# Optimization experiments

Hardware: AMD Instinct MI355X
Metric: run time of the kernel (lower is better)

The kernel has to match this reference:

```python
import jax, jax.numpy as jnp
import numpy as np

ALPHA = 0.2  # LeakyReLU negative slope
NEG_INF = -9e15  # matches torch -9000000000000000.0


def setup_inputs() -> dict:
    key = jax.random.key(0)
    k1, k2, k3, k4, k5, k6 = jax.random.split(key, 6)
    N, F_in, F_out = 4096, 512, 256
    adj = jax.random.randint(k1, (N, N), 0, 2, dtype=jnp.int32)
    h = jax.random.normal(k2, (N, F_in), dtype=jnp.float32)
    # proj: Linear(F_in, F_out)
    W = jax.random.normal(k3, (F_in, F_out), dtype=jnp.float32) * (1.0 / np.sqrt(F_in))
    b = jax.random.normal(k4, (F_out,), dtype=jnp.float32) * 0.01
    # proj_a: Linear(2*F_out, 1) split into the two halves acting on src/dst features
    a1 = jax.random.normal(k5, (F_out,), dtype=jnp.float32) * (1.0 / np.sqrt(2 * F_out))
    a2 = jax.random.normal(k6, (F_out,), dtype=jnp.float32) * (1.0 / np.sqrt(2 * F_out))
    a_b = jnp.zeros((), dtype=jnp.float32)
    return {"adj": adj, "h": h, "W": W, "b": b, "a1": a1, "a2": a2, "a_b": a_b}


def reference(adj, h, W, b, a1, a2, a_b):
    # wh = proj(h): [N, F_out]
    wh = h @ W + b
    # Fused form of the N x N x 2F concat + Linear(2F,1):
    # logits[i, j] = wh[i] . a1 + wh[j] . a2 + a_b
    f_src = wh @ a1  # [N]
    f_dst = wh @ a2  # [N]
    e = jax.nn.leaky_relu(f_src[:, None] + f_dst[None, :] + a_b, negative_slope=ALPHA)
    e = jnp.where(adj > 0, e, NEG_INF)
    att = jax.nn.softmax(e, axis=-1)  # F.softmax legacy dim=1 for 2D
    # dropout: inference mode (no-op) for deterministic reference
    out = att @ wh  # [N, F_out]
    return jax.nn.elu(out)  # concat=True
```

## Files before the change

kernel.cpp:

```cpp
#include <hip/hip_runtime.h>

#define NN   4096
#define FIN  512
#define FOUT 256
#define ALPHA 0.2f

typedef __attribute__((ext_vector_type(8))) short short8;
typedef __attribute__((ext_vector_type(4))) float f32x4;
typedef unsigned short u16;
typedef unsigned int u32;
typedef unsigned long long u64;

__device__ __forceinline__ u16 f2bf(float x) {
    union { float f; unsigned u; } v; v.f = x;
    unsigned r = v.u + 0x7FFF + ((v.u >> 16) & 1);
    return (u16)(r >> 16);
}

__global__ __launch_bounds__(256) void k_wt(const float* __restrict__ W,
                                            u16* __restrict__ Wt,
                                            float* __restrict__ fs,
                                            float* __restrict__ fd) {
    __shared__ float s[64 * 65];
    const int t  = threadIdx.x;
    const int g  = (blockIdx.y * gridDim.x + blockIdx.x) * 256 + t;
    if (g < NN) fs[g] = 0.f; else fd[g - NN] = 0.f;
    const int f0 = blockIdx.x * 64;
    const int k0 = blockIdx.y * 64;
    #pragma unroll
    for (int p = 0; p < 4; ++p) {
        int q = t + 256 * p, rr = q >> 4, cc = q & 15;
        float4 w4 = *(const float4*)&W[(size_t)(k0 + rr) * FOUT + f0 + cc * 4];
        s[(cc * 4 + 0) * 65 + rr] = w4.x;
        s[(cc * 4 + 1) * 65 + rr] = w4.y;
        s[(cc * 4 + 2) * 65 + rr] = w4.z;
        s[(cc * 4 + 3) * 65 + rr] = w4.w;
    }
    __syncthreads();
    #pragma unroll
    for (int p = 0; p < 4; ++p) {
        int q = t + 256 * p, f = q >> 4, kg = q & 15;
        ushort4 o;
        o.x = f2bf(s[f * 65 + kg * 4 + 0]);
        o.y = f2bf(s[f * 65 + kg * 4 + 1]);
        o.z = f2bf(s[f * 65 + kg * 4 + 2]);
        o.w = f2bf(s[f * 65 + kg * 4 + 3]);
        *(ushort4*)&Wt[(size_t)(f0 + f) * FIN + k0 + kg * 4] = o;
    }
}

#define HS 520
__global__ __launch_bounds__(256) void k_proj(const float* __restrict__ h,
                                              const u16* __restrict__ Wt,
                                              const float* __restrict__ bias,
                                              const float* __restrict__ a1,
                                              const float* __restrict__ a2,
                                              const int* __restrict__ adj,
                                              u16* __restrict__ whT,
                                              float* __restrict__ fs,
                                              float* __restrict__ fd,
                                              u64* __restrict__ bits) {
    __shared__ u16 s_h[32 * HS];
    const int t  = threadIdx.x;
    const int f0 = blockIdx.x * 64;
    const int i0 = blockIdx.y * 32;
    #pragma unroll
    for (int p = 0; p < 16; ++p) {
        int q = t + 256 * p, row = q >> 7, c4 = q & 127;
        float4 v = *(const float4*)&h[(size_t)(i0 + row) * FIN + c4 * 4];
        ushort4 o; o.x = f2bf(v.x); o.y = f2bf(v.y); o.z = f2bf(v.z); o.w = f2bf(v.w);
        *(ushort4*)&s_h[row * HS + c4 * 4] = o;
    }
    __syncthreads();
    const int w = t >> 6, l = t & 63, n = l & 15, quad = l >> 4;
    const int hh = w & 1, fh = w >> 1;
    f32x4 acc[2] = {{0.f,0.f,0.f,0.f},{0.f,0.f,0.f,0.f}};
    #pragma unroll
    for (int k0 = 0; k0 < FIN; k0 += 32) {
        short8 a = *(const short8*)&s_h[(hh * 16 + n) * HS + k0 + quad * 8];
        short8 b0 = *(const short8*)&Wt[(size_t)(f0 + fh * 32 + n) * FIN + k0 + quad * 8];
        short8 b1 = *(const short8*)&Wt[(size_t)(f0 + fh * 32 + 16 + n) * FIN + k0 + quad * 8];
        acc[0] = __builtin_amdgcn_mfma_f32_16x16x32_bf16(a, b0, acc[0], 0, 0, 0);
        acc[1] = __builtin_amdgcn_mfma_f32_16x16x32_bf16(a, b1, acc[1], 0, 0, 0);
    }
    const int fb = f0 + fh * 32 + n;
    const float bv0 = bias[fb],  bv1 = bias[fb + 16];
    const float a10 = a1[fb],    a11 = a1[fb + 16];
    const float a20 = a2[fb],    a21 = a2[fb + 16];
    u16* wt_tile = whT + (size_t)(i0 >> 5) * (FOUT * 32);
    float d1[4], d2[4];
    #pragma unroll
    for (int r = 0; r < 4; ++r) {
        const int ic = hh * 16 + quad * 4 + r;
        const float v0 = acc[0][r] + bv0;
        const float v1 = acc[1][r] + bv1;
        wt_tile[fb * 32 + ic]        = f2bf(v0);
        wt_tile[(fb + 16) * 32 + ic] = f2bf(v1);
        d1[r] = v0 * a10 + v1 * a11;
        d2[r] = v0 * a20 + v1 * a21;
    }
    #pragma unroll
    for (int m = 1; m < 16; m <<= 1) {
        #pragma unroll
        for (int r = 0; r < 4; ++r) {
            d1[r] += __shfl_xor(d1[r], m);
            d2[r] += __shfl_xor(d2[r], m);
        }
    }
    if (n == 0) {
        #pragma unroll
        for (int r = 0; r < 4; ++r) {
            const int i = i0 + hh * 16 + quad * 4 + r;
            atomicAdd(&fs[i], d1[r]);
            atomicAdd(&fd[i], d2[r]);
        }
    }
    {
        const int rr = i0 + (blockIdx.x << 3) + (w << 1);
        #pragma unroll
        for (int s = 0; s < 2; ++s) {
            const size_t ab = (size_t)(rr + s) * NN;
            u64* dst = bits + (size_t)(rr + s) * 64;
            #pragma unroll 2
            for (int o = 0; o < 16; ++o) {
                u64 q0 = __ballot(adj[ab + (o * 4 + 0) * 64 + l] > 0);
                u64 q1 = __ballot(adj[ab + (o * 4 + 1) * 64 + l] > 0);
                u64 q2 = __ballot(adj[ab + (o * 4 + 2) * 64 + l] > 0);
                u64 q3 = __ballot(adj[ab + (o * 4 + 3) * 64 + l] > 0);
                if (l == 0) {
                    dst[o * 4 + 0] = q0;
                    dst[o * 4 + 1] = q1;
                    dst[o * 4 + 2] = q2;
                    dst[o * 4 + 3] = q3;
                }
            }
        }
    }
}

#define BI 32
#define CJ 8

__device__ __forceinline__ void comp_step(
        const short8& b0, const short8& b1, const short8& b2, const short8& b3,
        const float* s_F, const float* s_H, int joff, int jq8,
        u32 w0, u32 w1, float E0, float G0, float E1, float G1,
        f32x4 (&acc)[2][4], float& rs0, float& rs1) {
    const float4 Fa = *(const float4*)&s_F[joff + jq8];
    const float4 Fb = *(const float4*)&s_F[joff + jq8 + 4];
    const float4 Ha = *(const float4*)&s_H[joff + jq8];
    const float4 Hb = *(const float4*)&s_H[joff + jq8 + 4];
    const u32 bw0 = w0 >> jq8, bw1 = w1 >> jq8;
    float q0, q1, q2, q3, q4, q5, q6, q7;
    u32 d0, d1, d2, d3;
    union { short8 v; u32 d[4]; } o0, o1;
#define PEL1(FV, HV, BW, K, E, G, RS, PP) do { \
        float _m = fmaxf((E) * (FV), (G) * (HV)); \
        PP = ((BW) & (1u << (K))) ? _m : 0.f; RS += PP; } while (0)
    PEL1(Fa.x, Ha.x, bw0, 0, E0, G0, rs0, q0);
    PEL1(Fa.y, Ha.y, bw0, 1, E0, G0, rs0, q1);
    PEL1(Fa.z, Ha.z, bw0, 2, E0, G0, rs0, q2);
    PEL1(Fa.w, Ha.w, bw0, 3, E0, G0, rs0, q3);
    PEL1(Fb.x, Hb.x, bw0, 4, E0, G0, rs0, q4);
    PEL1(Fb.y, Hb.y, bw0, 5, E0, G0, rs0, q5);
    PEL1(Fb.z, Hb.z, bw0, 6, E0, G0, rs0, q6);
    PEL1(Fb.w, Hb.w, bw0, 7, E0, G0, rs0, q7);
    asm("v_cvt_pk_bf16_f32 %0, %1, %2" : "=v"(d0) : "v"(q0), "v"(q1));
    asm("v_cvt_pk_bf16_f32 %0, %1, %2" : "=v"(d1) : "v"(q2), "v"(q3));
    asm("v_cvt_pk_bf16_f32 %0, %1, %2" : "=v"(d2) : "v"(q4), "v"(q5));
    asm("v_cvt_pk_bf16_f32 %0, %1, %2" : "=v"(d3) : "v"(q6), "v"(q7));
    o0.d[0] = d0; o0.d[1] = d1; o0.d[2] = d2; o0.d[3] = d3;
    PEL1(Fa.x, Ha.x, bw1, 0, E1, G1, rs1, q0);
    PEL1(Fa.y, Ha.y, bw1, 1, E1, G1, rs1, q1);
    PEL1(Fa.z, Ha.z, bw1, 2, E1, G1, rs1, q2);
    PEL1(Fa.w, Ha.w, bw1, 3, E1, G1, rs1, q3);
    PEL1(Fb.x, Hb.x, bw1, 4, E1, G1, rs1, q4);
    PEL1(Fb.y, Hb.y, bw1, 5, E1, G1, rs1, q5);
    PEL1(Fb.z, Hb.z, bw1, 6, E1, G1, rs1, q6);
    PEL1(Fb.w, Hb.w, bw1, 7, E1, G1, rs1, q7);
#undef PEL1
    asm("v_cvt_pk_bf16_f32 %0, %1, %2" : "=v"(d0) : "v"(q0), "v"(q1));
    asm("v_cvt_pk_bf16_f32 %0, %1, %2" : "=v"(d1) : "v"(q2), "v"(q3));
    asm("v_cvt_pk_bf16_f32 %0, %1, %2" : "=v"(d2) : "v"(q4), "v"(q5));
    asm("v_cvt_pk_bf16_f32 %0, %1, %2" : "=v"(d3) : "v"(q6), "v"(q7));
    o1.d[0] = d0; o1.d[1] = d1; o1.d[2] = d2; o1.d[3] = d3;
    __builtin_amdgcn_s_setprio(1);
    acc[0][0] = __builtin_amdgcn_mfma_f32_16x16x32_bf16(o0.v, b0, acc[0][0], 0, 0, 0);
    acc[0][1] = __builtin_amdgcn_mfma_f32_16x16x32_bf16(o0.v, b1, acc[0][1], 0, 0, 0);
    acc[0][2] = __builtin_amdgcn_mfma_f32_16x16x32_bf16(o0.v, b2, acc[0][2], 0, 0, 0);
    acc[0][3] = __builtin_amdgcn_mfma_f32_16x16x32_bf16(o0.v, b3, acc[0][3], 0, 0, 0);
    acc[1][0] = __builtin_amdgcn_mfma_f32_16x16x32_bf16(o1.v, b0, acc[1][0], 0, 0, 0);
    acc[1][1] = __builtin_amdgcn_mfma_f32_16x16x32_bf16(o1.v, b1, acc[1][1], 0, 0, 0);
    acc[1][2] = __builtin_amdgcn_mfma_f32_16x16x32_bf16(o1.v, b2, acc[1][2], 0, 0, 0);
    acc[1][3] = __builtin_amdgcn_mfma_f32_16x16x32_bf16(o1.v, b3, acc[1][3], 0, 0, 0);
    __builtin_amdgcn_s_setprio(0);
}

__global__ __launch_bounds__(256) void k_attn(const u32* __restrict__ bits,
                                              const u16* __restrict__ whT,
                                              const float* __restrict__ fs,
                                              const float* __restrict__ fd,
                                              const float* __restrict__ ab,
                                              float* __restrict__ part,
                                              float* __restrict__ psum) {
    __shared__ float s_F[NN / CJ], s_H[NN / CJ];
    const int t = threadIdx.x;
    const int w = t >> 6, l = t & 63, n = l & 15, quad = l >> 4;
    const int i0 = blockIdx.x * BI;
    const int c  = blockIdx.y;
    const int jbeg = c * (NN / CJ), jend = jbeg + (NN / CJ);
    const int fw  = w * 64;
    const int jq8 = quad * 8;

    const float abv = ab[0];
    const float s0 = fs[i0 + n] + abv;
    const float s1 = fs[i0 + 16 + n] + abv;
    const float E0 = __expf(s0), G0 = __expf(ALPHA * s0);
    const float E1 = __expf(s1), G1 = __expf(ALPHA * s1);

    const u32* B0 = bits + (size_t)(i0 + n) * 128;
    const u32* B1 = bits + (size_t)(i0 + 16 + n) * 128;
    uint4 m0 = *(const uint4*)&B0[jbeg >> 5];
    uint4 m1 = *(const uint4*)&B1[jbeg >> 5];

    short8 Ab0, Ab1, Ab2, Ab3, Bb0, Bb1, Bb2, Bb3;
#define LDB(P, J0) do { const u16* tb_ = whT + (size_t)((J0) >> 5) * (FOUT * 32) + quad * 8; \
        P##0 = *(const short8*)&tb_[(fw + n) * 32]; \
        P##1 = *(const short8*)&tb_[(fw + n + 16) * 32]; \
        P##2 = *(const short8*)&tb_[(fw + n + 32) * 32]; \
        P##3 = *(const short8*)&tb_[(fw + n + 48) * 32]; } while (0)

    LDB(Ab, jbeg);

    if (t < 128) {
        float4 v = *(const float4*)&fd[jbeg + t * 4];
        float4 F, H;
        F.x = __expf(v.x); F.y = __expf(v.y); F.z = __expf(v.z); F.w = __expf(v.w);
        H.x = __expf(ALPHA * v.x); H.y = __expf(ALPHA * v.y);
        H.z = __expf(ALPHA * v.z); H.w = __expf(ALPHA * v.w);
        *(float4*)&s_F[t * 4] = F;
        *(float4*)&s_H[t * 4] = H;
    }
    __syncthreads();

    f32x4 acc[2][4] = {{{0.f,0.f,0.f,0.f},{0.f,0.f,0.f,0.f},{0.f,0.f,0.f,0.f},{0.f,0.f,0.f,0.f}},
                       {{0.f,0.f,0.f,0.f},{0.f,0.f,0.f,0.f},{0.f,0.f,0.f,0.f},{0.f,0.f,0.f,0.f}}};
    float rs0 = 0.f, rs1 = 0.f;

    #pragma unroll 1
    for (int jb = jbeg; jb < jend; jb += 128) {
        const uint4 cm0 = m0, cm1 = m1;
        if (jb + 128 < jend) {
            m0 = *(const uint4*)&B0[(jb + 128) >> 5];
            m1 = *(const uint4*)&B1[(jb + 128) >> 5];
        }
        LDB(Bb, jb + 32);
        comp_step(Ab0, Ab1, Ab2, Ab3, s_F, s_H, jb - jbeg,      jq8, cm0.x, cm1.x, E0, G0, E1, G1, acc, rs0, rs1);
        LDB(Ab, jb + 64);
        comp_step(Bb0, Bb1, Bb2, Bb3, s_F, s_H, jb - jbeg + 32, jq8, cm0.y, cm1.y, E0, G0, E1, G1, acc, rs0, rs1);
        LDB(Bb, jb + 96);
        comp_step(Ab0, Ab1, Ab2, Ab3, s_F, s_H, jb - jbeg + 64, jq8, cm0.z, cm1.z, E0, G0, E1, G1, acc, rs0, rs1);
        if (jb + 128 < jend) LDB(Ab, jb + 128);
        comp_step(Bb0, Bb1, Bb2, Bb3, s_F, s_H, jb - jbeg + 96, jq8, cm0.w, cm1.w, E0, G0, E1, G1, acc, rs0, rs1);
    }
#undef LDB
    rs0 += __shfl_xor(rs0, 16); rs0 += __shfl_xor(rs0, 32);
    rs1 += __shfl_xor(rs1, 16); rs1 += __shfl_xor(rs1, 32);
    if (w == 0 && quad == 0) {
        psum[(size_t)c * NN + i0 + n]      = rs0;
        psum[(size_t)c * NN + i0 + 16 + n] = rs1;
    }
    float* pc = part + ((size_t)c * NN + i0) * FOUT;
    #pragma unroll
    for (int hf = 0; hf < 2; ++hf)
        #pragma unroll
        for (int u = 0; u < 4; ++u)
            #pragma unroll
            for (int r = 0; r < 4; ++r)
                pc[(size_t)(hf * 16 + quad * 4 + r) * FOUT + fw + u * 16 + n] = acc[hf][u][r];
}

__global__ __launch_bounds__(256) void k_fin(const float* __restrict__ part,
                                             const float* __restrict__ psum,
                                             float* __restrict__ out, int C) {
    const int g = blockIdx.x * 256 + threadIdx.x;
    const int i = g >> 6;
    const size_t s4 = (size_t)NN * FOUT / 4;
    float4 a = ((const float4*)part)[g];
    float s = psum[i];
    for (int c = 1; c < C; ++c) {
        float4 bb = ((const float4*)part)[g + (size_t)c * s4];
        a.x += bb.x; a.y += bb.y; a.z += bb.z; a.w += bb.w;
        s += psum[(size_t)c * NN + i];
    }
    const float inv = 1.0f / s;
    a.x *= inv; a.y *= inv; a.z *= inv; a.w *= inv;
    a.x = a.x > 0.f ? a.x : __expf(a.x) - 1.f;
    a.y = a.y > 0.f ? a.y : __expf(a.y) - 1.f;
    a.z = a.z > 0.f ? a.z : __expf(a.z) - 1.f;
    a.w = a.w > 0.f ? a.w : __expf(a.w) - 1.f;
    ((float4*)out)[g] = a;
}

extern "C" void kernel_launch(void* const* d_in, const int* in_sizes, int n_in,
                              void* d_out, int out_size, void* d_ws, size_t ws_size,
                              hipStream_t stream) {
    const int*   adj = (const int*)  d_in[0];
    const float* h   = (const float*)d_in[1];
    const float* W   = (const float*)d_in[2];
    const float* b   = (const float*)d_in[3];
    const float* a1  = (const float*)d_in[4];
    const float* a2  = (const float*)d_in[5];
    const float* ab  = (const float*)d_in[6];
    float* out = (float*)d_out;

    const int C = CJ;

    float* fs   = (float*)d_ws;
    float* fd   = fs + NN;
    float* psum = fd + NN;
    float* part = psum + (size_t)C * NN;
    u16*   Wt   = (u16*)(part + (size_t)C * NN * FOUT);
    u16*   whT  = Wt + (size_t)FOUT * FIN;
    u64*   bits = (u64*)(whT + (size_t)NN * FOUT);

    k_wt  <<<dim3(FOUT / 64, FIN / 64), 256, 0, stream>>>(W, Wt, fs, fd);
    k_proj<<<dim3(FOUT / 64, NN / 32), 256, 0, stream>>>(h, Wt, b, a1, a2, adj, whT, fs, fd, bits);
    k_attn<<<dim3(NN / BI, CJ), 256, 0, stream>>>((const u32*)bits, whT, fs, fd, ab, part, psum);
    k_fin <<<(NN * FOUT / 4) / 256, 256, 0, stream>>>(part, psum, out, C);
}
```

Measured before the change: 167.8 us.

## Split adjacency bit-packing into separate blocks of the projection kernel

```diff
diff --git a/kernel.cpp b/kernel.cpp
--- a/kernel.cpp
+++ b/kernel.cpp
@@ -50,20 +50,42 @@
 }
 
 #define HS 520
-__global__ __launch_bounds__(256) void k_proj(const float* __restrict__ h,
-                                              const u16* __restrict__ Wt,
-                                              const float* __restrict__ bias,
-                                              const float* __restrict__ a1,
-                                              const float* __restrict__ a2,
-                                              const int* __restrict__ adj,
-                                              u16* __restrict__ whT,
-                                              float* __restrict__ fs,
-                                              float* __restrict__ fd,
-                                              u64* __restrict__ bits) {
+__global__ __launch_bounds__(256) void k_pb(const float* __restrict__ h,
+                                            const u16* __restrict__ Wt,
+                                            const float* __restrict__ bias,
+                                            const float* __restrict__ a1,
+                                            const float* __restrict__ a2,
+                                            const int* __restrict__ adj,
+                                            u16* __restrict__ whT,
+                                            float* __restrict__ fs,
+                                            float* __restrict__ fd,
+                                            u64* __restrict__ bits) {
     __shared__ u16 s_h[32 * HS];
-    const int t  = threadIdx.x;
-    const int f0 = blockIdx.x * 64;
-    const int i0 = blockIdx.y * 32;
+    const int bid = blockIdx.x;
+    const int t   = threadIdx.x;
+    if (bid >= 512) {
+        const int l = t & 63, wv = t >> 6;
+        const int row  = (bid - 512) * 2 + (wv >> 1);
+        const int half = wv & 1;
+        const size_t base = (size_t)row * NN + half * 2048;
+        u64* dst = bits + (size_t)row * 64 + half * 32;
+        #pragma unroll
+        for (int o = 0; o < 8; ++o) {
+            u64 b0 = __ballot(adj[base + (o * 4 + 0) * 64 + l] > 0);
+            u64 b1 = __ballot(adj[base + (o * 4 + 1) * 64 + l] > 0);
+            u64 b2 = __ballot(adj[base + (o * 4 + 2) * 64 + l] > 0);
+            u64 b3 = __ballot(adj[base + (o * 4 + 3) * 64 + l] > 0);
+            if (l == 0) {
+                dst[o * 4 + 0] = b0;
+                dst[o * 4 + 1] = b1;
+                dst[o * 4 + 2] = b2;
+                dst[o * 4 + 3] = b3;
+            }
+        }
+        return;
+    }
+    const int f0 = (bid & 3) * 64;
+    const int i0 = (bid >> 2) * 32;
     #pragma unroll
     for (int p = 0; p < 16; ++p) {
         int q = t + 256 * p, row = q >> 7, c4 = q & 127;
@@ -113,27 +135,6 @@
             const int i = i0 + hh * 16 + quad * 4 + r;
             atomicAdd(&fs[i], d1[r]);
             atomicAdd(&fd[i], d2[r]);
-        }
-    }
-    {
-        const int rr = i0 + (blockIdx.x << 3) + (w << 1);
-        #pragma unroll
-        for (int s = 0; s < 2; ++s) {
-            const size_t ab = (size_t)(rr + s) * NN;
-            u64* dst = bits + (size_t)(rr + s) * 64;
-            #pragma unroll 2
-            for (int o = 0; o < 16; ++o) {
-                u64 q0 = __ballot(adj[ab + (o * 4 + 0) * 64 + l] > 0);
-                u64 q1 = __ballot(adj[ab + (o * 4 + 1) * 64 + l] > 0);
-                u64 q2 = __ballot(adj[ab + (o * 4 + 2) * 64 + l] > 0);
-                u64 q3 = __ballot(adj[ab + (o * 4 + 3) * 64 + l] > 0);
-                if (l == 0) {
-                    dst[o * 4 + 0] = q0;
-                    dst[o * 4 + 1] = q1;
-                    dst[o * 4 + 2] = q2;
-                    dst[o * 4 + 3] = q3;
-                }
-            }
         }
     }
 }
@@ -325,7 +326,7 @@
     u64*   bits = (u64*)(whT + (size_t)NN * FOUT);
 
     k_wt  <<<dim3(FOUT / 64, FIN / 64), 256, 0, stream>>>(W, Wt, fs, fd);
-    k_proj<<<dim3(FOUT / 64, NN / 32), 256, 0, stream>>>(h, Wt, b, a1, a2, adj, whT, fs, fd, bits);
+    k_pb  <<<512 + NN / 2, 256, 0, stream>>>(h, Wt, b, a1, a2, adj, whT, fs, fd, bits);
     k_attn<<<dim3(NN / BI, CJ), 256, 0, stream>>>((const u32*)bits, whT, fs, fd, ab, part, psum);
     k_fin <<<(NN * FOUT / 4) / 256, 256, 0, stream>>>(part, psum, out, C);
 }
```

Result: faster. 154.4 us (-8.0%).
